# Kernel optimization log

Measured on AMD Instinct MI355X. Metric: run time of the kernel, lower is better.

The kernel has to match this reference:

```python
import jax, jax.numpy as jnp
import numpy as np

B, C, D, O = 4, 4096, 1024, 1024
PROJ = 256
RANKS = [1, 2, 4, 8]
E = len(RANKS)
CLAMP_MAX = float(np.log(1.0 / 0.01))  # log(100)


def setup_inputs() -> dict:
    key = jax.random.key(0)
    ks = jax.random.split(key, 16)
    inp = {
        "x": jax.random.normal(ks[0], (B, C, D), dtype=jnp.float32),
        "W": jax.random.normal(ks[1], (O, D), dtype=jnp.float32) / np.sqrt(D),
        "Wp": jax.random.normal(ks[2], (PROJ, D), dtype=jnp.float32) / np.sqrt(D),
        "bp": jnp.zeros((PROJ,), dtype=jnp.float32),
        "sim": jax.random.normal(ks[3], (PROJ, E), dtype=jnp.float32) * 0.01,
        "temp": jnp.full((1,), np.log(1.0 / 0.5), dtype=jnp.float32),
    }
    for i, r in enumerate(RANKS):
        inp[f"Wd{i}"] = jax.random.normal(ks[4 + 2 * i], (r, D), dtype=jnp.float32) / r
        inp[f"Wu{i}"] = jax.random.normal(ks[5 + 2 * i], (O, r), dtype=jnp.float32) * 0.01
    return inp


def _l2norm(v, axis):
    return v / jnp.maximum(jnp.linalg.norm(v, axis=axis, keepdims=True), 1e-12)


def reference(x, W, Wp, bp, sim, temp, Wd0, Wu0, Wd1, Wu1, Wd2, Wu2, Wd3, Wu3):
    # base linear (bias=False)
    base = jnp.einsum("bcd,od->bco", x, W)

    # cosine top-k gate on flattened tokens
    xf = x.reshape(-1, x.shape[-1])                         # [N, D]
    proj = _l2norm(xf @ Wp.T + bp, axis=1)                  # [N, PROJ]
    simn = _l2norm(sim, axis=0)                             # [PROJ, E]
    scale = jnp.exp(jnp.minimum(temp, CLAMP_MAX))
    logits = (proj @ simn) * scale                          # [N, E]

    # eval mode: no noise. softmax then top-1 mask * prob
    lw = jax.nn.softmax(logits, axis=1)
    top1 = jnp.argmax(lw, axis=1)                           # [N]
    ret = jnp.where(jnp.arange(E)[None, :] == top1[:, None], lw, 0.0)
    ret = ret.reshape(x.shape[0], x.shape[1], E)            # [B, C, E]

    # dense per-expert LoRA (ranks differ, so small fixed loop)
    downs = (Wd0, Wd1, Wd2, Wd3)
    ups = (Wu0, Wu1, Wu2, Wu3)
    l = jnp.stack(
        [jnp.einsum("bcr,or->bco", jnp.einsum("bcd,rd->bcr", x, d), u)
         for d, u in zip(downs, ups)],
        axis=2,
    )                                                       # [B, C, E, O]
    res = jnp.sum(ret[..., None] * l, axis=2)               # [B, C, O]
    return base + res
```

## Files before the change

### kernel.cpp

```cpp
#include <hip/hip_runtime.h>

#define TOK 16384
#define DD 1024
#define OO 1024
#define KE 1088
#define NT 17
#define NB1 288
#define CLAMPV 4.605170185988091f

typedef __attribute__((ext_vector_type(8))) short short8;
typedef __attribute__((ext_vector_type(4))) float f32x4;
typedef __attribute__((ext_vector_type(2))) unsigned int uint2e;
typedef __attribute__((ext_vector_type(4))) unsigned int uint4e;

__device__ __forceinline__ unsigned short f2bf(float f) {
  unsigned int u = __float_as_uint(f);
  return (unsigned short)((u + 0x7FFFu + ((u >> 16) & 1u)) >> 16);
}

__device__ __forceinline__ void gload16(const unsigned short* g, unsigned short* l) {
  __builtin_amdgcn_global_load_lds(
      (const __attribute__((address_space(1))) void*)g,
      (__attribute__((address_space(3))) void*)l, 16, 0, 0);
}

__device__ __forceinline__ float down_val(int j, int d,
    const float* __restrict__ Wd0, const float* __restrict__ Wd1,
    const float* __restrict__ Wd2, const float* __restrict__ Wd3) {
  if (j == 0) return Wd0[d];
  if (j < 3) return Wd1[(j - 1) * DD + d];
  if (j < 7) return Wd2[(j - 3) * DD + d];
  if (j < 15) return Wd3[(j - 7) * DD + d];
  return 0.f;
}

__global__ __launch_bounds__(256) void prep3(
    const float* __restrict__ W, const float* __restrict__ Wp,
    const float* __restrict__ sim, const float* __restrict__ bp,
    const float* __restrict__ Wd0, const float* __restrict__ Wd1,
    const float* __restrict__ Wd2, const float* __restrict__ Wd3,
    const float* __restrict__ Wu0, const float* __restrict__ Wu1,
    const float* __restrict__ Wu2, const float* __restrict__ Wu3,
    unsigned short* __restrict__ Bx, unsigned short* __restrict__ B1,
    unsigned short* __restrict__ Ax, float* __restrict__ v4,
    float* __restrict__ c4) {
  __shared__ float simn_l[256][4];
  __shared__ float part[4][4];
  const int tid = threadIdx.x;
  if (blockIdx.x < 4) {
    float4 sv = *(const float4*)&sim[tid * 4];
    float v[4] = {sv.x * sv.x, sv.y * sv.y, sv.z * sv.z, sv.w * sv.w};
#pragma unroll
    for (int off = 1; off < 64; off <<= 1) {
#pragma unroll
      for (int e = 0; e < 4; ++e) v[e] += __shfl_xor(v[e], off, 64);
    }
    int wv = tid >> 6, ln = tid & 63;
    if (ln == 0) { part[wv][0] = v[0]; part[wv][1] = v[1]; part[wv][2] = v[2]; part[wv][3] = v[3]; }
    __syncthreads();
    float n0 = fmaxf(sqrtf(part[0][0] + part[1][0] + part[2][0] + part[3][0]), 1e-12f);
    float n1 = fmaxf(sqrtf(part[0][1] + part[1][1] + part[2][1] + part[3][1]), 1e-12f);
    float n2 = fmaxf(sqrtf(part[0][2] + part[1][2] + part[2][2] + part[3][2]), 1e-12f);
    float n3 = fmaxf(sqrtf(part[0][3] + part[1][3] + part[2][3] + part[3][3]), 1e-12f);
    simn_l[tid][0] = sv.x / n0; simn_l[tid][1] = sv.y / n1;
    simn_l[tid][2] = sv.z / n2; simn_l[tid][3] = sv.w / n3;
    __syncthreads();
    int d = blockIdx.x * 256 + tid;
    float a0 = 0.f, a1 = 0.f, a2 = 0.f, a3 = 0.f;
    for (int j = 0; j < 256; ++j) {
      float w = Wp[j * DD + d];
      a0 = __builtin_fmaf(w, simn_l[j][0], a0);
      a1 = __builtin_fmaf(w, simn_l[j][1], a1);
      a2 = __builtin_fmaf(w, simn_l[j][2], a2);
      a3 = __builtin_fmaf(w, simn_l[j][3], a3);
    }
    v4[d] = a0; v4[1024 + d] = a1; v4[2048 + d] = a2; v4[3072 + d] = a3;
    if (blockIdx.x == 0) {
      float bpv = bp[tid];
      float pc[4] = {simn_l[tid][0] * bpv, simn_l[tid][1] * bpv,
                     simn_l[tid][2] * bpv, simn_l[tid][3] * bpv};
#pragma unroll
      for (int off = 1; off < 64; off <<= 1) {
#pragma unroll
        for (int e = 0; e < 4; ++e) pc[e] += __shfl_xor(pc[e], off, 64);
      }
      __syncthreads();
      if (ln == 0) { part[wv][0] = pc[0]; part[wv][1] = pc[1]; part[wv][2] = pc[2]; part[wv][3] = pc[3]; }
      __syncthreads();
      if (tid == 0) {
#pragma unroll
        for (int e = 0; e < 4; ++e)
          c4[e] = part[0][e] + part[1][e] + part[2][e] + part[3][e];
      }
    }
  }
  const int nB1 = 16 * NB1 * 64;
  const int nWb = OO * KE;
  const int nXpad = TOK * 48;
  const int total = nB1 + nWb + nXpad;
  for (int i = blockIdx.x * 256 + tid; i < total; i += gridDim.x * 256) {
    if (i < nB1) {
      int kt = i / (NB1 * 64);
      int rem = i - kt * (NB1 * 64);
      int r = rem >> 6, kk = rem & 63;
      int k = kt * 64 + (kk ^ ((r & 7) << 3));
      float v = 0.f;
      if (r < 256) v = Wp[r * DD + k];
      else if (r < 271) v = down_val(r - 256, k, Wd0, Wd1, Wd2, Wd3);
      B1[i] = f2bf(v);
    } else if (i < nB1 + nWb) {
      int j = i - nB1;
      int o = j / KE, c = j - o * KE;
      float v = 0.f;
      if (c < 1024) v = W[o * DD + c];
      else if (c == 1024) v = Wu0[o];
      else if (c < 1027) v = Wu1[o * 2 + (c - 1025)];
      else if (c < 1031) v = Wu2[o * 4 + (c - 1027)];
      else if (c < 1039) v = Wu3[o * 8 + (c - 1031)];
      Bx[j] = f2bf(v);
    } else {
      int j = i - nB1 - nWb;
      int row = j / 48, c = j - row * 48;
      Ax[row * KE + 1040 + c] = 0;
    }
  }
}

__global__ __launch_bounds__(256, 2) void gemm2f(
    const float* __restrict__ x, const float* __restrict__ v4,
    unsigned short* __restrict__ Ax, const unsigned short* __restrict__ B1L,
    const float* __restrict__ c4, const float* __restrict__ bp,
    const float* __restrict__ temp) {
  __shared__ __align__(16) unsigned short as1[2][32 * 64];
  __shared__ __align__(16) unsigned short bs1[2][NB1 * 64];
  const int tid = threadIdx.x;
  const int lane = tid & 63, wv = tid >> 6;
  const int wm = wv >> 1, wn = wv & 1;
  const int r0 = blockIdx.x * 32;
  const int ro = lane & 15;
  const int rswz = (ro & 7) << 3;
  const int xr = tid >> 3;
  const int xc = (tid & 7) * 4;
  const int aswz = (xr & 7) << 3;
  const float* xgp = &x[(r0 + xr) * DD + xc];
  unsigned short* axp = &Ax[(r0 + xr) * KE + xc];
  f32x4 acc[9] = {};
  float dotp[4] = {};

#define STB1(KT, BUF)                                                         \
  for (int c = wv; c < 36; c += 4)                                            \
    gload16(&B1L[(KT) * (NB1 * 64) + c * 512 + lane * 8], &bs1[BUF][c * 512]);

#define XSTG(KT, BUF)                                                         \
  _Pragma("unroll")                                                           \
  for (int h = 0; h < 2; ++h) {                                               \
    float4 xv = *(const float4*)(xgp + (KT) * 64 + h * 32);                   \
    float4 va = *(const float4*)&v4[(KT) * 64 + h * 32 + xc];                 \
    float4 vb = *(const float4*)&v4[1024 + (KT) * 64 + h * 32 + xc];          \
    float4 vc = *(const float4*)&v4[2048 + (KT) * 64 + h * 32 + xc];          \
    float4 vd = *(const float4*)&v4[3072 + (KT) * 64 + h * 32 + xc];          \
    dotp[0] = __builtin_fmaf(xv.x, va.x, __builtin_fmaf(xv.y, va.y,           \
              __builtin_fmaf(xv.z, va.z, __builtin_fmaf(xv.w, va.w, dotp[0])))); \
    dotp[1] = __builtin_fmaf(xv.x, vb.x, __builtin_fmaf(xv.y, vb.y,           \
              __builtin_fmaf(xv.z, vb.z, __builtin_fmaf(xv.w, vb.w, dotp[1])))); \
    dotp[2] = __builtin_fmaf(xv.x, vc.x, __builtin_fmaf(xv.y, vc.y,           \
              __builtin_fmaf(xv.z, vc.z, __builtin_fmaf(xv.w, vc.w, dotp[2])))); \
    dotp[3] = __builtin_fmaf(xv.x, vd.x, __builtin_fmaf(xv.y, vd.y,           \
              __builtin_fmaf(xv.z, vd.z, __builtin_fmaf(xv.w, vd.w, dotp[3])))); \
    union { unsigned short s[4]; uint2e q; } pk;                              \
    pk.s[0] = f2bf(xv.x); pk.s[1] = f2bf(xv.y);                               \
    pk.s[2] = f2bf(xv.z); pk.s[3] = f2bf(xv.w);                               \
    __builtin_nontemporal_store(pk.q,                                         \
        reinterpret_cast<uint2e*>(axp + (KT) * 64 + h * 32));                 \
    *reinterpret_cast<uint2e*>(                                               \
        &as1[BUF][xr * 64 + (((h << 5) + xc) ^ aswz)]) = pk.q;                \
  }

#define MM(BUF)                                                               \
  _Pragma("unroll")                                                           \
  for (int kh = 0; kh < 2; ++kh) {                                            \
    const int kb = ((kh << 5) + ((lane >> 4) << 3)) ^ rswz;                   \
    short8 af = *reinterpret_cast<const short8*>(                             \
        &as1[BUF][(wm * 16 + ro) * 64 + kb]);                                 \
    _Pragma("unroll")                                                         \
    for (int n = 0; n < 9; ++n) {                                             \
      short8 bf = *reinterpret_cast<const short8*>(                           \
          &bs1[BUF][(wn * 144 + n * 16 + ro) * 64 + kb]);                     \
      acc[n] = __builtin_amdgcn_mfma_f32_16x16x32_bf16(af, bf, acc[n], 0, 0, 0); \
    }                                                                         \
  }

  STB1(0, 0)
  XSTG(0, 0)
  __syncthreads();
  int cur = 0;
  for (int u = 0; u < 16; ++u) {
    if (u < 15) {
      STB1(u + 1, cur ^ 1)
      XSTG(u + 1, cur ^ 1)
    }
    MM(cur)
    if (u < 15) {
      __syncthreads();
      cur ^= 1;
    }
  }
  __syncthreads();

  float* eps = (float*)&bs1[0][0];
  float* ssq_s = eps;
  float* xdown_s = eps + 64;
  float* dots_s = eps + 576;

#pragma unroll
  for (int off = 1; off < 8; off <<= 1) {
#pragma unroll
    for (int e = 0; e < 4; ++e) dotp[e] += __shfl_xor(dotp[e], off, 64);
  }
  if ((lane & 7) == 0) {
    dots_s[xr * 4 + 0] = dotp[0]; dots_s[xr * 4 + 1] = dotp[1];
    dots_s[xr * 4 + 2] = dotp[2]; dots_s[xr * 4 + 3] = dotp[3];
  }

  float ssqp[4] = {};
#pragma unroll
  for (int n = 0; n < 9; ++n) {
    int col = wn * 144 + n * 16 + ro;
    if (col < 256) {
      float b = bp[col];
#pragma unroll
      for (int r = 0; r < 4; ++r) {
        float a = acc[n][r] + b;
        ssqp[r] = __builtin_fmaf(a, a, ssqp[r]);
      }
    }
  }
#pragma unroll
  for (int off = 1; off < 16; off <<= 1) {
#pragma unroll
    for (int r = 0; r < 4; ++r) ssqp[r] += __shfl_xor(ssqp[r], off, 64);
  }
  if (ro == 0) {
#pragma unroll
    for (int r = 0; r < 4; ++r)
      ssq_s[wn * 32 + wm * 16 + (lane >> 4) * 4 + r] = ssqp[r];
  }
  if (wn == 1 && ro < 15) {
#pragma unroll
    for (int r = 0; r < 4; ++r)
      xdown_s[(wm * 16 + (lane >> 4) * 4 + r) * 16 + ro] = acc[7][r];
  }
  __syncthreads();

  if (tid < 32) {
    const int row = tid, t = r0 + row;
    float ssqT = ssq_s[row] + ssq_s[32 + row];
    float4 cc = *reinterpret_cast<const float4*>(c4);
    float scale = expf(fminf(temp[0], CLAMPV));
    float inv = scale / fmaxf(sqrtf(ssqT), 1e-12f);
    float l[4];
    l[0] = (dots_s[row * 4 + 0] + cc.x) * inv; l[1] = (dots_s[row * 4 + 1] + cc.y) * inv;
    l[2] = (dots_s[row * 4 + 2] + cc.z) * inv; l[3] = (dots_s[row * 4 + 3] + cc.w) * inv;
    int be = 0; float m = l[0];
    if (l[1] > m) { m = l[1]; be = 1; }
    if (l[2] > m) { m = l[2]; be = 2; }
    if (l[3] > m) { m = l[3]; be = 3; }
    float den = expf(l[0] - m) + expf(l[1] - m) + expf(l[2] - m) + expf(l[3] - m);
    float g = 1.0f / den;
    int off = (1 << be) - 1;
    int rr = 1 << be;
    union { unsigned short s[16]; uint4e v[2]; } o;
#pragma unroll
    for (int j = 0; j < 16; ++j) {
      float dv = xdown_s[row * 16 + (j & 15)];
      float v = (j >= off && j < off + rr) ? g * dv : 0.f;
      o.s[j] = f2bf(v);
    }
    uint4e* dst = reinterpret_cast<uint4e*>(&Ax[t * KE + 1024]);
    __builtin_nontemporal_store(o.v[0], dst);
    __builtin_nontemporal_store(o.v[1], dst + 1);
  }
#undef STB1
#undef XSTG
#undef MM
}

__global__ __launch_bounds__(512, 2) void main_gemm8(
    const unsigned short* __restrict__ A, const unsigned short* __restrict__ Bm,
    float* __restrict__ C) {
  __shared__ __align__(16) unsigned short lbuf[2][32768];
  const int tid = threadIdx.x;
  const int lane = tid & 63, wv = tid >> 6;
  const int wm = wv >> 2, wn = wv & 3;
  const int dd = blockIdx.x;
  const int tt = (dd & 7) * 32 + (dd >> 3);
  const int bx = tt & 3, by = tt >> 2;
  const int r0 = by * 256, c0 = bx * 256;
  const int ro = lane & 15, ko = (lane >> 4) * 8;
  const int rowb = ro * 128;
  const int swz = (ro & 7) << 4;
  const int lk0 = (ko * 2) ^ swz;
  const int lk1 = (64 + ko * 2) ^ swz;
  const int ll = (lane * 16) ^ ((lane >> 3) << 4);
  const int sro = ll >> 7;
  const int sk = (ll & 127) >> 1;
  f32x4 acc[8][4] = {};
  short8 Af[4][2], B0[2][2], B1r[2][2];

#define STG(MTX, GRB, HBU, BUF, U2)                                           \
  do {                                                                        \
    gload16(&MTX[((GRB) + (0 * 8 + wv) * 8 + sro) * KE + (U2) * 64 + sk],     \
            &lbuf[BUF][(HBU) + (0 * 8 + wv) * 512]);                          \
    gload16(&MTX[((GRB) + (1 * 8 + wv) * 8 + sro) * KE + (U2) * 64 + sk],     \
            &lbuf[BUF][(HBU) + (1 * 8 + wv) * 512]);                          \
  } while (0)

#define LDA(FI, QM, LK) (*reinterpret_cast<const short8*>(                    \
    (const char*)Ab + wm * 16384 + (QM) * 8192 + (FI) * 2048 + rowb + (LK)))
#define LDB(FN, QN, LK) (*reinterpret_cast<const short8*>(                    \
    (const char*)Bb + wn * 8192 + (QN) * 4096 + (FN) * 2048 + rowb + (LK)))

#define MMQ(QM, QN, BF)                                                       \
  do {                                                                        \
    _Pragma("unroll")                                                         \
    for (int fi = 0; fi < 4; ++fi) {                                          \
      _Pragma("unroll")                                                       \
      for (int fn = 0; fn < 2; ++fn) {                                        \
        acc[(QM)*4+fi][(QN)*2+fn] = __builtin_amdgcn_mfma_f32_16x16x32_bf16(  \
            Af[fi][0], BF[fn][0], acc[(QM)*4+fi][(QN)*2+fn], 0, 0, 0);        \
        acc[(QM)*4+fi][(QN)*2+fn] = __builtin_amdgcn_mfma_f32_16x16x32_bf16(  \
            Af[fi][1], BF[fn][1], acc[(QM)*4+fi][(QN)*2+fn], 0, 0, 0);        \
      }                                                                       \
    }                                                                         \
  } while (0)

  STG(Bm, c0,       16384, 0, 0);
  STG(A,  r0,       0,     0, 0);
  STG(Bm, c0 + 128, 24576, 0, 0);
  STG(A,  r0 + 128, 8192,  0, 0);
  STG(Bm, c0,       16384, 1, 1);
  STG(A,  r0,       0,     1, 1);
  asm volatile("s_waitcnt vmcnt(4)" ::: "memory");
  __builtin_amdgcn_s_barrier();

  for (int u = 0; u < NT; ++u) {
    const int db = u & 1;
    const unsigned short* Ab = &lbuf[db][0];
    const unsigned short* Bb = &lbuf[db][16384];
#pragma unroll
    for (int fi = 0; fi < 4; ++fi) { Af[fi][0] = LDA(fi, 0, lk0); Af[fi][1] = LDA(fi, 0, lk1); }
#pragma unroll
    for (int fn = 0; fn < 2; ++fn) { B0[fn][0] = LDB(fn, 0, lk0); B0[fn][1] = LDB(fn, 0, lk1); }
    if (u + 1 < NT) STG(Bm, c0 + 128, 24576, (u + 1) & 1, u + 1);
    __builtin_amdgcn_s_barrier();
    __builtin_amdgcn_s_setprio(1);
    MMQ(0, 0, B0);
    __builtin_amdgcn_s_setprio(0);
    __builtin_amdgcn_s_barrier();
#pragma unroll
    for (int fn = 0; fn < 2; ++fn) { B1r[fn][0] = LDB(fn, 1, lk0); B1r[fn][1] = LDB(fn, 1, lk1); }
    if (u + 1 < NT) STG(A, r0 + 128, 8192, (u + 1) & 1, u + 1);
    __builtin_amdgcn_s_barrier();
    __builtin_amdgcn_s_setprio(1);
    MMQ(0, 1, B1r);
    __builtin_amdgcn_s_setprio(0);
    __builtin_amdgcn_s_barrier();
#pragma unroll
    for (int fi = 0; fi < 4; ++fi) { Af[fi][0] = LDA(fi, 1, lk0); Af[fi][1] = LDA(fi, 1, lk1); }
    if (u + 2 < NT) STG(Bm, c0, 16384, db, u + 2);
    __builtin_amdgcn_s_barrier();
    __builtin_amdgcn_s_setprio(1);
    MMQ(1, 1, B1r);
    __builtin_amdgcn_s_setprio(0);
    __builtin_amdgcn_s_barrier();
    if (u + 2 < NT) STG(A, r0, 0, db, u + 2);
    __builtin_amdgcn_s_barrier();
    __builtin_amdgcn_s_setprio(1);
    MMQ(1, 0, B0);
    __builtin_amdgcn_s_setprio(0);
    if (u + 2 < NT) {
      asm volatile("s_waitcnt vmcnt(4)" ::: "memory");
    } else if (u == NT - 2) {
      asm volatile("s_waitcnt vmcnt(0)" ::: "memory");
    }
    __builtin_amdgcn_s_barrier();
  }

#pragma unroll
  for (int m = 0; m < 8; ++m) {
    int rr = r0 + wm * 128 + m * 16 + (lane >> 4) * 4;
#pragma unroll
    for (int n = 0; n < 4; ++n) {
      int cc = c0 + wn * 64 + n * 16 + ro;
#pragma unroll
      for (int v = 0; v < 4; ++v)
        C[(rr + v) * OO + cc] = acc[m][n][v];
    }
  }
#undef STG
#undef LDA
#undef LDB
#undef MMQ
}

extern "C" void kernel_launch(void* const* d_in, const int* in_sizes, int n_in,
                              void* d_out, int out_size, void* d_ws, size_t ws_size,
                              hipStream_t stream) {
  const float* x    = (const float*)d_in[0];
  const float* W    = (const float*)d_in[1];
  const float* Wp   = (const float*)d_in[2];
  const float* bp   = (const float*)d_in[3];
  const float* sim  = (const float*)d_in[4];
  const float* temp = (const float*)d_in[5];
  const float* Wd0  = (const float*)d_in[6];
  const float* Wu0  = (const float*)d_in[7];
  const float* Wd1  = (const float*)d_in[8];
  const float* Wu1  = (const float*)d_in[9];
  const float* Wd2  = (const float*)d_in[10];
  const float* Wu2  = (const float*)d_in[11];
  const float* Wd3  = (const float*)d_in[12];
  const float* Wu3  = (const float*)d_in[13];
  float* out = (float*)d_out;
  char* ws = (char*)d_ws;
  unsigned short* Ax  = (unsigned short*)ws;
  unsigned short* Bx  = (unsigned short*)(ws + 35651584);
  unsigned short* B1L = (unsigned short*)(ws + 37879808);
  float* v4           = (float*)(ws + 38469632);
  float* c4           = (float*)(ws + 38486016);

  prep3<<<1024, 256, 0, stream>>>(W, Wp, sim, bp, Wd0, Wd1, Wd2, Wd3,
                                  Wu0, Wu1, Wu2, Wu3, Bx, B1L, Ax, v4, c4);
  gemm2f<<<512, 256, 0, stream>>>(x, v4, Ax, B1L, c4, bp, temp);
  main_gemm8<<<256, 512, 0, stream>>>(Ax, Bx, out);
}
```

Measured before the change: 96.76 us.

## Process 64 rows per block in gate GEMM to reuse staged weight tiles

```diff
diff --git a/kernel.cpp b/kernel.cpp
--- a/kernel.cpp
+++ b/kernel.cpp
@@ -126,17 +126,17 @@
   }
 }
 
-__global__ __launch_bounds__(256, 2) void gemm2f(
+__global__ __launch_bounds__(256, 1) void gemm4f(
     const float* __restrict__ x, const float* __restrict__ v4,
     unsigned short* __restrict__ Ax, const unsigned short* __restrict__ B1L,
     const float* __restrict__ c4, const float* __restrict__ bp,
     const float* __restrict__ temp) {
-  __shared__ __align__(16) unsigned short as1[2][32 * 64];
+  __shared__ __align__(16) unsigned short as1[2][2][32 * 64];
   __shared__ __align__(16) unsigned short bs1[2][NB1 * 64];
   const int tid = threadIdx.x;
   const int lane = tid & 63, wv = tid >> 6;
   const int wm = wv >> 1, wn = wv & 1;
-  const int r0 = blockIdx.x * 32;
+  const int r0 = blockIdx.x * 64;
   const int ro = lane & 15;
   const int rswz = (ro & 7) << 3;
   const int xr = tid >> 3;
@@ -144,62 +144,66 @@
   const int aswz = (xr & 7) << 3;
   const float* xgp = &x[(r0 + xr) * DD + xc];
   unsigned short* axp = &Ax[(r0 + xr) * KE + xc];
-  f32x4 acc[9] = {};
-  float dotp[4] = {};
+  f32x4 acc[2][9] = {};
+  float dotp[2][4] = {};
 
 #define STB1(KT, BUF)                                                         \
   for (int c = wv; c < 36; c += 4)                                            \
     gload16(&B1L[(KT) * (NB1 * 64) + c * 512 + lane * 8], &bs1[BUF][c * 512]);
 
-#define XSTG(KT, BUF)                                                         \
+#define XSTG(KT, RT, BUF)                                                     \
   _Pragma("unroll")                                                           \
   for (int h = 0; h < 2; ++h) {                                               \
-    float4 xv = *(const float4*)(xgp + (KT) * 64 + h * 32);                   \
+    float4 xv = *(const float4*)(xgp + (RT) * 32 * DD + (KT) * 64 + h * 32);  \
     float4 va = *(const float4*)&v4[(KT) * 64 + h * 32 + xc];                 \
     float4 vb = *(const float4*)&v4[1024 + (KT) * 64 + h * 32 + xc];          \
     float4 vc = *(const float4*)&v4[2048 + (KT) * 64 + h * 32 + xc];          \
     float4 vd = *(const float4*)&v4[3072 + (KT) * 64 + h * 32 + xc];          \
-    dotp[0] = __builtin_fmaf(xv.x, va.x, __builtin_fmaf(xv.y, va.y,           \
-              __builtin_fmaf(xv.z, va.z, __builtin_fmaf(xv.w, va.w, dotp[0])))); \
-    dotp[1] = __builtin_fmaf(xv.x, vb.x, __builtin_fmaf(xv.y, vb.y,           \
-              __builtin_fmaf(xv.z, vb.z, __builtin_fmaf(xv.w, vb.w, dotp[1])))); \
-    dotp[2] = __builtin_fmaf(xv.x, vc.x, __builtin_fmaf(xv.y, vc.y,           \
-              __builtin_fmaf(xv.z, vc.z, __builtin_fmaf(xv.w, vc.w, dotp[2])))); \
-    dotp[3] = __builtin_fmaf(xv.x, vd.x, __builtin_fmaf(xv.y, vd.y,           \
-              __builtin_fmaf(xv.z, vd.z, __builtin_fmaf(xv.w, vd.w, dotp[3])))); \
+    dotp[RT][0] = __builtin_fmaf(xv.x, va.x, __builtin_fmaf(xv.y, va.y,       \
+        __builtin_fmaf(xv.z, va.z, __builtin_fmaf(xv.w, va.w, dotp[RT][0])))); \
+    dotp[RT][1] = __builtin_fmaf(xv.x, vb.x, __builtin_fmaf(xv.y, vb.y,       \
+        __builtin_fmaf(xv.z, vb.z, __builtin_fmaf(xv.w, vb.w, dotp[RT][1])))); \
+    dotp[RT][2] = __builtin_fmaf(xv.x, vc.x, __builtin_fmaf(xv.y, vc.y,       \
+        __builtin_fmaf(xv.z, vc.z, __builtin_fmaf(xv.w, vc.w, dotp[RT][2])))); \
+    dotp[RT][3] = __builtin_fmaf(xv.x, vd.x, __builtin_fmaf(xv.y, vd.y,       \
+        __builtin_fmaf(xv.z, vd.z, __builtin_fmaf(xv.w, vd.w, dotp[RT][3])))); \
     union { unsigned short s[4]; uint2e q; } pk;                              \
     pk.s[0] = f2bf(xv.x); pk.s[1] = f2bf(xv.y);                               \
     pk.s[2] = f2bf(xv.z); pk.s[3] = f2bf(xv.w);                               \
-    __builtin_nontemporal_store(pk.q,                                         \
-        reinterpret_cast<uint2e*>(axp + (KT) * 64 + h * 32));                 \
+    *reinterpret_cast<uint2e*>(axp + (RT) * 32 * KE + (KT) * 64 + h * 32) = pk.q; \
     *reinterpret_cast<uint2e*>(                                               \
-        &as1[BUF][xr * 64 + (((h << 5) + xc) ^ aswz)]) = pk.q;                \
-  }
-
-#define MM(BUF)                                                               \
+        &as1[BUF][RT][xr * 64 + (((h << 5) + xc) ^ aswz)]) = pk.q;            \
+  }
+
+#define MM2(BUF)                                                              \
   _Pragma("unroll")                                                           \
   for (int kh = 0; kh < 2; ++kh) {                                            \
     const int kb = ((kh << 5) + ((lane >> 4) << 3)) ^ rswz;                   \
-    short8 af = *reinterpret_cast<const short8*>(                             \
-        &as1[BUF][(wm * 16 + ro) * 64 + kb]);                                 \
+    short8 af0 = *reinterpret_cast<const short8*>(                            \
+        &as1[BUF][0][(wm * 16 + ro) * 64 + kb]);                              \
+    short8 af1 = *reinterpret_cast<const short8*>(                            \
+        &as1[BUF][1][(wm * 16 + ro) * 64 + kb]);                              \
     _Pragma("unroll")                                                         \
     for (int n = 0; n < 9; ++n) {                                             \
       short8 bf = *reinterpret_cast<const short8*>(                           \
           &bs1[BUF][(wn * 144 + n * 16 + ro) * 64 + kb]);                     \
-      acc[n] = __builtin_amdgcn_mfma_f32_16x16x32_bf16(af, bf, acc[n], 0, 0, 0); \
+      acc[0][n] = __builtin_amdgcn_mfma_f32_16x16x32_bf16(af0, bf, acc[0][n], 0, 0, 0); \
+      acc[1][n] = __builtin_amdgcn_mfma_f32_16x16x32_bf16(af1, bf, acc[1][n], 0, 0, 0); \
     }                                                                         \
   }
 
   STB1(0, 0)
-  XSTG(0, 0)
+  XSTG(0, 0, 0)
+  XSTG(0, 1, 0)
   __syncthreads();
   int cur = 0;
   for (int u = 0; u < 16; ++u) {
     if (u < 15) {
       STB1(u + 1, cur ^ 1)
-      XSTG(u + 1, cur ^ 1)
-    }
-    MM(cur)
+      XSTG(u + 1, 0, cur ^ 1)
+      XSTG(u + 1, 1, cur ^ 1)
+    }
+    MM2(cur)
     if (u < 15) {
       __syncthreads();
       cur ^= 1;
@@ -209,52 +213,67 @@
 
   float* eps = (float*)&bs1[0][0];
   float* ssq_s = eps;
-  float* xdown_s = eps + 64;
-  float* dots_s = eps + 576;
+  float* xdown_s = eps + 128;
+  float* dots_s = eps + 1152;
 
 #pragma unroll
   for (int off = 1; off < 8; off <<= 1) {
 #pragma unroll
-    for (int e = 0; e < 4; ++e) dotp[e] += __shfl_xor(dotp[e], off, 64);
+    for (int rt = 0; rt < 2; ++rt)
+#pragma unroll
+      for (int e = 0; e < 4; ++e) dotp[rt][e] += __shfl_xor(dotp[rt][e], off, 64);
   }
   if ((lane & 7) == 0) {
-    dots_s[xr * 4 + 0] = dotp[0]; dots_s[xr * 4 + 1] = dotp[1];
-    dots_s[xr * 4 + 2] = dotp[2]; dots_s[xr * 4 + 3] = dotp[3];
-  }
-
-  float ssqp[4] = {};
+#pragma unroll
+    for (int rt = 0; rt < 2; ++rt) {
+      dots_s[(rt * 32 + xr) * 4 + 0] = dotp[rt][0];
+      dots_s[(rt * 32 + xr) * 4 + 1] = dotp[rt][1];
+      dots_s[(rt * 32 + xr) * 4 + 2] = dotp[rt][2];
+      dots_s[(rt * 32 + xr) * 4 + 3] = dotp[rt][3];
+    }
+  }
+
+  float ssqp[2][4] = {};
 #pragma unroll
   for (int n = 0; n < 9; ++n) {
     int col = wn * 144 + n * 16 + ro;
     if (col < 256) {
       float b = bp[col];
 #pragma unroll
-      for (int r = 0; r < 4; ++r) {
-        float a = acc[n][r] + b;
-        ssqp[r] = __builtin_fmaf(a, a, ssqp[r]);
-      }
+      for (int rt = 0; rt < 2; ++rt)
+#pragma unroll
+        for (int r = 0; r < 4; ++r) {
+          float a = acc[rt][n][r] + b;
+          ssqp[rt][r] = __builtin_fmaf(a, a, ssqp[rt][r]);
+        }
     }
   }
 #pragma unroll
   for (int off = 1; off < 16; off <<= 1) {
 #pragma unroll
-    for (int r = 0; r < 4; ++r) ssqp[r] += __shfl_xor(ssqp[r], off, 64);
+    for (int rt = 0; rt < 2; ++rt)
+#pragma unroll
+      for (int r = 0; r < 4; ++r) ssqp[rt][r] += __shfl_xor(ssqp[rt][r], off, 64);
   }
   if (ro == 0) {
 #pragma unroll
-    for (int r = 0; r < 4; ++r)
-      ssq_s[wn * 32 + wm * 16 + (lane >> 4) * 4 + r] = ssqp[r];
+    for (int rt = 0; rt < 2; ++rt)
+#pragma unroll
+      for (int r = 0; r < 4; ++r)
+        ssq_s[wn * 64 + rt * 32 + wm * 16 + (lane >> 4) * 4 + r] = ssqp[rt][r];
   }
   if (wn == 1 && ro < 15) {
 #pragma unroll
-    for (int r = 0; r < 4; ++r)
-      xdown_s[(wm * 16 + (lane >> 4) * 4 + r) * 16 + ro] = acc[7][r];
+    for (int rt = 0; rt < 2; ++rt)
+#pragma unroll
+      for (int r = 0; r < 4; ++r)
+        xdown_s[(rt * 32 + wm * 16 + (lane >> 4) * 4 + r) * 16 + ro] = acc[rt][7][r];
   }
   __syncthreads();
 
-  if (tid < 32) {
+  if (tid < 64) {
     const int row = tid, t = r0 + row;
-    float ssqT = ssq_s[row] + ssq_s[32 + row];
+    float ssqT = ssq_s[row] + ssq_s[64 + row];
     float4 cc = *reinterpret_cast<const float4*>(c4);
     float scale = expf(fminf(temp[0], CLAMPV));
     float inv = scale / fmaxf(sqrtf(ssqT), 1e-12f);
@@ -277,12 +296,12 @@
       o.s[j] = f2bf(v);
     }
     uint4e* dst = reinterpret_cast<uint4e*>(&Ax[t * KE + 1024]);
-    __builtin_nontemporal_store(o.v[0], dst);
-    __builtin_nontemporal_store(o.v[1], dst + 1);
+    dst[0] = o.v[0];
+    dst[1] = o.v[1];
   }
 #undef STB1
 #undef XSTG
-#undef MM
+#undef MM2
 }
 
 __global__ __launch_bounds__(512, 2) void main_gemm8(
@@ -430,6 +449,6 @@
 
   prep3<<<1024, 256, 0, stream>>>(W, Wp, sim, bp, Wd0, Wd1, Wd2, Wd3,
                                   Wu0, Wu1, Wu2, Wu3, Bx, B1L, Ax, v4, c4);
-  gemm2f<<<512, 256, 0, stream>>>(x, v4, Ax, B1L, c4, bp, temp);
+  gemm4f<<<256, 256, 0, stream>>>(x, v4, Ax, B1L, c4, bp, temp);
   main_gemm8<<<256, 512, 0, stream>>>(Ax, Bx, out);
 }
```

Measured after the change: 97.12 us. No clear change (+0.4%).
